# Performance work log

Hardware: AMD Instinct MI355X
Metric: run time of the kernel (lower is better)

The kernel has to match this reference:

```python
import jax, jax.numpy as jnp
import numpy as np

N = 100000
E = 3200000
IN_DIM = 256
HID = 64
NC = 32
K1 = 2  # conv1 propagation steps
EPS = 1e-5


def setup_inputs() -> dict:
    key = jax.random.key(0)
    ks = jax.random.split(key, 8)
    x = jax.random.normal(ks[0], (N, IN_DIM), dtype=jnp.float32)
    src = jax.random.randint(ks[1], (E,), 0, N)
    dst = jax.random.randint(ks[2], (E,), 0, N)
    W1 = jax.random.normal(ks[3], (IN_DIM, HID), dtype=jnp.float32) / np.sqrt(IN_DIM)
    b1 = jnp.zeros((HID,), dtype=jnp.float32)
    gamma = jnp.ones((HID,), dtype=jnp.float32)
    beta = jnp.zeros((HID,), dtype=jnp.float32)
    W2 = jax.random.normal(ks[4], (HID, NC), dtype=jnp.float32) / np.sqrt(HID)
    b2 = jnp.zeros((NC,), dtype=jnp.float32)
    return {"x": x, "src": src, "dst": dst, "W1": W1, "b1": b1,
            "gamma": gamma, "beta": beta, "W2": W2, "b2": b2}


def _gcn_norm(src, dst, n):
    # deg includes self loop (add_self_loops=True): deg[i] = 1 + in-degree
    deg = jax.ops.segment_sum(jnp.ones_like(src, dtype=jnp.float32), dst, num_segments=n) + 1.0
    dinv = jax.lax.rsqrt(deg)
    w_edge = dinv[src] * dinv[dst]      # [E] normalized edge weights
    w_self = dinv * dinv                # [N] self-loop weights (1/deg)
    return w_edge, w_self


def _propagate(h, src, dst, w_edge, w_self, n):
    # out = D^-1/2 (A+I) D^-1/2 h  via gather-scale-scatter
    msg = w_edge[:, None] * h[src]
    agg = jax.ops.segment_sum(msg, dst, num_segments=n)
    return agg + w_self[:, None] * h


def reference(x, src, dst, W1, b1, gamma, beta, W2, b2):
    n = x.shape[0]
    w_edge, w_self = _gcn_norm(src, dst, n)
    # conv1: K-step propagation then linear
    h = x
    for _ in range(K1):
        h = _propagate(h, src, dst, w_edge, w_self, n)
    h = h @ W1 + b1
    # batchnorm (training-mode batch stats over nodes, biased variance)
    mean = jnp.mean(h, axis=0)
    var = jnp.mean(jnp.square(h - mean), axis=0)
    h = (h - mean) * jax.lax.rsqrt(var + EPS) * gamma + beta
    h = jax.nn.selu(h)
    # dropout p=0.0 -> identity
    # conv2: 1-step propagation then linear
    h = _propagate(h, src, dst, w_edge, w_self, n)
    h = h @ W2 + b2
    return jax.nn.log_softmax(h, axis=1)
```

## Files before the change

### kernel.cpp

```cpp
#include <hip/hip_runtime.h>
#include <hip/hip_fp16.h>

#define NN 100000
#define EE 3200000
#define NB 256
#define NPB 391
#define NBLK_A 512
#define CHUNK_A (EE / NBLK_A)

#define OFF_AF   0UL
#define OFF_AH   25600000UL
#define OFF_BH   38400000UL
#define OFF_CNT  (OFF_BH + 65536UL)
#define OFF_LOC  (OFF_CNT + 524288UL)
#define OFF_CSR  51200000UL
#define OFF_RP   64000000UL
#define OFF_DINV 64400384UL
#define OFF_BASE 64808960UL
#define OFF_BN   64813056UL
#define OFF_SS   64813568UL

typedef __attribute__((ext_vector_type(8))) short bf16x8;
typedef __attribute__((ext_vector_type(4))) float f32x4;

__global__ __launch_bounds__(256) void passA2(const int* __restrict__ src, const int* __restrict__ dst,
                                              int* __restrict__ cnt, int* __restrict__ loc,
                                              unsigned* __restrict__ gbuf) {
    __shared__ unsigned ebuf[CHUNK_A];
    __shared__ int hist[NB], cur[NB], sc[NB];
    int t = threadIdx.x, b = blockIdx.x;
    hist[t] = 0;
    __syncthreads();
    int beg = b * CHUNK_A;
    for (int i = t; i < CHUNK_A; i += 256)
        atomicAdd(&hist[dst[beg + i] / NPB], 1);
    __syncthreads();
    int h = hist[t];
    sc[t] = h;
    __syncthreads();
    for (int off = 1; off < 256; off <<= 1) {
        int v = (t >= off) ? sc[t - off] : 0;
        __syncthreads();
        sc[t] += v;
        __syncthreads();
    }
    int ex = sc[t] - h;
    cur[t] = ex;
    loc[b * NB + t] = ex;
    cnt[b * NB + t] = h;
    __syncthreads();
    for (int i = t; i < CHUNK_A; i += 256) {
        int d = dst[beg + i];
        int k = d / NPB;
        int dl = d - k * NPB;
        int p = atomicAdd(&cur[k], 1);
        ebuf[p] = ((unsigned)dl << 17) | (unsigned)src[beg + i];
    }
    __syncthreads();
    for (int i = t; i < CHUNK_A; i += 256)
        gbuf[beg + i] = ebuf[i];
}

__global__ __launch_bounds__(256) void basescan(const int* __restrict__ cnt, int* __restrict__ base,
                                                int* __restrict__ rp) {
    __shared__ int s[256];
    int t = threadIdx.x;
    int v = 0;
    for (int b = 0; b < NBLK_A; ++b) v += cnt[b * NB + t];
    s[t] = v;
    __syncthreads();
    for (int off = 1; off < 256; off <<= 1) {
        int u = (t >= off) ? s[t - off] : 0;
        __syncthreads();
        s[t] += u;
        __syncthreads();
    }
    base[t] = s[t] - v;
    if (t == 255) { base[256] = s[255]; rp[NN] = s[255]; }
}

__global__ __launch_bounds__(512) void passB2(const unsigned* __restrict__ gbuf,
                                              const int* __restrict__ cnt, const int* __restrict__ loc,
                                              const int* __restrict__ base,
                                              int* __restrict__ rp, float* __restrict__ dinv,
                                              int* __restrict__ csr) {
    __shared__ int deg_l[NPB];
    __shared__ int off_l[NPB];
    __shared__ int s[512];
    int k = blockIdx.x, t = threadIdx.x;
    for (int i = t; i < NPB; i += 512) deg_l[i] = 0;
    __syncthreads();
    int n  = cnt[t * NB + k];
    int so = t * CHUNK_A + loc[t * NB + k];
    for (int e = 0; e < n; ++e)
        atomicAdd(&deg_l[gbuf[so + e] >> 17], 1);
    __syncthreads();
    int d0 = (t < NPB) ? deg_l[t] : 0;
    s[t] = d0;
    __syncthreads();
    for (int off = 1; off < 512; off <<= 1) {
        int v = (t >= off) ? s[t - off] : 0;
        __syncthreads();
        s[t] += v;
        __syncthreads();
    }
    if (t < NPB) off_l[t] = s[t] - d0;
    __syncthreads();
    int nodebase = k * NPB;
    int cbase = base[k];
    for (int i = t; i < NPB; i += 512) {
        int node = nodebase + i;
        if (node < NN) {
            rp[node] = cbase + off_l[i];
            dinv[node] = rsqrtf((float)deg_l[i] + 1.0f);
        }
    }
    __syncthreads();
    for (int e = 0; e < n; ++e) {
        unsigned v = gbuf[so + e];
        int p = atomicAdd(&off_l[v >> 17], 1);
        csr[cbase + p] = (int)(v & 0x1FFFFu);
    }
}

__global__ __launch_bounds__(256) void wprep(const float* __restrict__ W1, short* __restrict__ wf) {
    int e = blockIdx.x * 256 + threadIdx.x;
    if (e >= 16384) return;
    int j = e & 7, lane = (e >> 3) & 63, nt = (e >> 9) & 3, ks = e >> 11;
    int k = ks * 32 + (lane >> 4) * 8 + j;
    int col = nt * 16 + (lane & 15);
    float w = W1[k * 64 + col];
    unsigned b = __float_as_uint(w);
    short hi = (short)(b >> 16);
    float hf = __uint_as_float(b & 0xFFFF0000u);
    float lo = w - hf;
    short lov = (short)(__float_as_uint(lo) >> 16);
    wf[((size_t)(ks * 8 + nt * 2 + 0) * 64 + lane) * 8 + j] = hi;
    wf[((size_t)(ks * 8 + nt * 2 + 1) * 64 + lane) * 8 + j] = lov;
}

__global__ __launch_bounds__(256) void gemm1(const float* __restrict__ x, const short* __restrict__ wf,
                                             const float* __restrict__ dinv, __half* __restrict__ Ah) {
    int wid = threadIdx.x >> 6, lane = threadIdx.x & 63;
    int g = blockIdx.x * 4 + wid;
    if (g >= NN / 16) return;
    int lrow = g * 16 + (lane & 15);
    int kgrp = (lane >> 4) * 8;
    const float* xp = x + (size_t)lrow * 256 + kgrp;
    f32x4 acc[4];
    #pragma unroll
    for (int nt = 0; nt < 4; ++nt) acc[nt] = (f32x4){0.f, 0.f, 0.f, 0.f};
    for (int ks = 0; ks < 8; ++ks) {
        float4 f0 = *(const float4*)(xp + ks * 32);
        float4 f1 = *(const float4*)(xp + ks * 32 + 4);
        bf16x8 a_hi, a_lo;
        const float* fp = &f0.x;
        #pragma unroll
        for (int j = 0; j < 8; ++j) {
            float f = (j < 4) ? fp[j] : (&f1.x)[j - 4];
            unsigned b = __float_as_uint(f);
            a_hi[j] = (short)(b >> 16);
            float lo = f - __uint_as_float(b & 0xFFFF0000u);
            a_lo[j] = (short)(__float_as_uint(lo) >> 16);
        }
        const short* wfk = wf + (size_t)(ks * 8) * 64 * 8;
        #pragma unroll
        for (int nt = 0; nt < 4; ++nt) {
            bf16x8 b_hi = *(const bf16x8*)(wfk + ((nt * 2 + 0) * 64 + lane) * 8);
            bf16x8 b_lo = *(const bf16x8*)(wfk + ((nt * 2 + 1) * 64 + lane) * 8);
            acc[nt] = __builtin_amdgcn_mfma_f32_16x16x32_bf16(a_hi, b_hi, acc[nt], 0, 0, 0);
            acc[nt] = __builtin_amdgcn_mfma_f32_16x16x32_bf16(a_hi, b_lo, acc[nt], 0, 0, 0);
            acc[nt] = __builtin_amdgcn_mfma_f32_16x16x32_bf16(a_lo, b_hi, acc[nt], 0, 0, 0);
        }
    }
    int mb = (lane >> 4) * 4;
    #pragma unroll
    for (int reg = 0; reg < 4; ++reg) {
        int row = g * 16 + mb + reg;
        float dv = dinv[row];
        #pragma unroll
        for (int nt = 0; nt < 4; ++nt)
            Ah[(size_t)row * 64 + nt * 16 + (lane & 15)] = __float2half(acc[nt][reg] * dv);
    }
}

template <int P>
__global__ __launch_bounds__(256) void agg64h(const __half* __restrict__ h, __half* __restrict__ outp,
                                              const int* __restrict__ rp, const int* __restrict__ csr,
                                              const float* __restrict__ dinv) {
    int lane = threadIdx.x & 63;
    int node = (blockIdx.x << 2) + (threadIdx.x >> 6);
    if (node >= NN) return;
    int hid = lane >> 5;
    int c2 = (lane & 31) * 2;
    float dd = dinv[node];
    float sfx = 0.f, sfy = 0.f;
    if (hid == 0) {
        __half2 sv = *(const __half2*)(h + (size_t)node * 64 + c2);
        sfx = __half2float(sv.x); sfy = __half2float(sv.y);
    }
    __half2 haccA = __float2half2_rn(0.f);
    __half2 haccB = __float2half2_rn(0.f);
    int beg = rp[node], end = rp[node + 1];
    for (int j0 = beg; j0 < end; j0 += 64) {
        int m = end - j0; if (m > 64) m = 64;
        int s = csr[j0 + (lane < m ? lane : 0)];
        int j = 0;
        for (; j + 15 < m; j += 16) {
            int i0 = __shfl(s, j + hid);
            int i1 = __shfl(s, j + 2 + hid);
            int i2 = __shfl(s, j + 4 + hid);
            int i3 = __shfl(s, j + 6 + hid);
            int i4 = __shfl(s, j + 8 + hid);
            int i5 = __shfl(s, j + 10 + hid);
            int i6 = __shfl(s, j + 12 + hid);
            int i7 = __shfl(s, j + 14 + hid);
            __half2 v0 = *(const __half2*)(h + (size_t)i0 * 64 + c2);
            __half2 v1 = *(const __half2*)(h + (size_t)i1 * 64 + c2);
            __half2 v2 = *(const __half2*)(h + (size_t)i2 * 64 + c2);
            __half2 v3 = *(const __half2*)(h + (size_t)i3 * 64 + c2);
            __half2 v4 = *(const __half2*)(h + (size_t)i4 * 64 + c2);
            __half2 v5 = *(const __half2*)(h + (size_t)i5 * 64 + c2);
            __half2 v6 = *(const __half2*)(h + (size_t)i6 * 64 + c2);
            __half2 v7 = *(const __half2*)(h + (size_t)i7 * 64 + c2);
            __half2 tA = __hadd2(__hadd2(v0, v2), __hadd2(v4, v6));
            __half2 tB = __hadd2(__hadd2(v1, v3), __hadd2(v5, v7));
            haccA = __hadd2(haccA, tA);
            haccB = __hadd2(haccB, tB);
        }
        for (; j + 7 < m; j += 8) {
            int i0 = __shfl(s, j + hid);
            int i1 = __shfl(s, j + 2 + hid);
            int i2 = __shfl(s, j + 4 + hid);
            int i3 = __shfl(s, j + 6 + hid);
            __half2 v0 = *(const __half2*)(h + (size_t)i0 * 64 + c2);
            __half2 v1 = *(const __half2*)(h + (size_t)i1 * 64 + c2);
            __half2 v2 = *(const __half2*)(h + (size_t)i2 * 64 + c2);
            __half2 v3 = *(const __half2*)(h + (size_t)i3 * 64 + c2);
            haccA = __hadd2(haccA, __hadd2(v0, v2));
            haccB = __hadd2(haccB, __hadd2(v1, v3));
        }
        for (; j < m; j += 2) {
            int idx = j + hid;
            int cidx = idx < m ? idx : m - 1;
            int sj = __shfl(s, cidx);
            if (idx < m) {
                __half2 v = *(const __half2*)(h + (size_t)sj * 64 + c2);
                haccA = __hadd2(haccA, v);
            }
        }
    }
    float2 fA = __half22float2(haccA);
    float2 fB = __half22float2(haccB);
    float sx = sfx + fA.x + fB.x;
    float sy = sfy + fA.y + fB.y;
    sx += __shfl(sx, lane ^ 32);
    sy += __shfl(sy, lane ^ 32);
    if (hid == 0) {
        float w = (P == 2) ? dd * dd : dd;
        __half2 o;
        o.x = __float2half(sx * w); o.y = __float2half(sy * w);
        *(__half2*)(outp + (size_t)node * 64 + c2) = o;
    }
}

__global__ __launch_bounds__(256) void agg32f(const __half* __restrict__ U, float* __restrict__ outp,
                                              const int* __restrict__ rp, const int* __restrict__ csr,
                                              const float* __restrict__ dinv, const float* __restrict__ b2) {
    int lane = threadIdx.x & 63;
    int node = (blockIdx.x << 2) + (threadIdx.x >> 6);
    if (node >= NN) return;
    int gid = lane >> 4;
    int c2 = (lane & 15) * 2;
    float dd = dinv[node];
    float sfx = 0.f, sfy = 0.f;
    if (gid == 0) {
        __half2 sv = *(const __half2*)(U + (size_t)node * 32 + c2);
        sfx = __half2float(sv.x); sfy = __half2float(sv.y);
    }
    __half2 hacc = __float2half2_rn(0.f);
    int beg = rp[node], end = rp[node + 1];
    for (int j0 = beg; j0 < end; j0 += 64) {
        int m = end - j0; if (m > 64) m = 64;
        int s = csr[j0 + (lane < m ? lane : 0)];
        int j = 0;
        for (; j + 15 < m; j += 16) {
            int i0 = __shfl(s, j + gid);
            int i1 = __shfl(s, j + 4 + gid);
            int i2 = __shfl(s, j + 8 + gid);
            int i3 = __shfl(s, j + 12 + gid);
            __half2 v0 = *(const __half2*)(U + (size_t)i0 * 32 + c2);
            __half2 v1 = *(const __half2*)(U + (size_t)i1 * 32 + c2);
            __half2 v2 = *(const __half2*)(U + (size_t)i2 * 32 + c2);
            __half2 v3 = *(const __half2*)(U + (size_t)i3 * 32 + c2);
            hacc = __hadd2(hacc, __hadd2(__hadd2(v0, v1), __hadd2(v2, v3)));
        }
        for (; j + 7 < m; j += 8) {
            int i0 = __shfl(s, j + gid);
            int i1 = __shfl(s, j + 4 + gid);
            __half2 v0 = *(const __half2*)(U + (size_t)i0 * 32 + c2);
            __half2 v1 = *(const __half2*)(U + (size_t)i1 * 32 + c2);
            hacc = __hadd2(hacc, __hadd2(v0, v1));
        }
        for (; j < m; j += 4) {
            int idx = j + gid;
            int cidx = idx < m ? idx : m - 1;
            int sj = __shfl(s, cidx);
            if (idx < m) {
                __half2 v = *(const __half2*)(U + (size_t)sj * 32 + c2);
                hacc = __hadd2(hacc, v);
            }
        }
    }
    float2 fh = __half22float2(hacc);
    float ax = sfx + fh.x, ay = sfy + fh.y;
    ax += __shfl(ax, lane ^ 16); ay += __shfl(ay, lane ^ 16);
    ax += __shfl(ax, lane ^ 32); ay += __shfl(ay, lane ^ 32);
    float v0 = ax * dd + b2[c2];
    float v1 = ay * dd + b2[c2 + 1];
    float mx = fmaxf(v0, v1);
    mx = fmaxf(mx, __shfl_xor(mx, 1));
    mx = fmaxf(mx, __shfl_xor(mx, 2));
    mx = fmaxf(mx, __shfl_xor(mx, 4));
    mx = fmaxf(mx, __shfl_xor(mx, 8));
    float sum = __expf(v0 - mx) + __expf(v1 - mx);
    sum += __shfl_xor(sum, 1);
    sum += __shfl_xor(sum, 2);
    sum += __shfl_xor(sum, 4);
    sum += __shfl_xor(sum, 8);
    if (gid == 0) {
        float ls = __logf(sum);
        *(float2*)(outp + (size_t)node * 32 + c2) = make_float2(v0 - mx - ls, v1 - mx - ls);
    }
}

__global__ __launch_bounds__(256) void bn_stats(const __half* __restrict__ A, float* __restrict__ bn) {
    int t = threadIdx.x;
    int c = t & 63, rg = t >> 6;
    float s = 0.f, sq = 0.f;
    for (int r = blockIdx.x * 4 + rg; r < NN; r += gridDim.x * 4) {
        float v = __half2float(A[(size_t)r * 64 + c]);
        s += v; sq += v * v;
    }
    __shared__ float ls[256], lq[256];
    ls[t] = s; lq[t] = sq;
    __syncthreads();
    if (t < 64) {
        float S = ls[t] + ls[t + 64] + ls[t + 128] + ls[t + 192];
        float Q = lq[t] + lq[t + 64] + lq[t + 128] + lq[t + 192];
        atomicAdd(&bn[t], S);
        atomicAdd(&bn[64 + t], Q);
    }
}

__global__ void bn_final(const float* __restrict__ bn, const float* __restrict__ gamma,
                         const float* __restrict__ beta, float* __restrict__ ss) {
    int c = threadIdx.x;
    float mean = bn[c] / (float)NN;
    float var = bn[64 + c] / (float)NN - mean * mean;
    float sc = gamma[c] * rsqrtf(var + 1e-5f);
    ss[c] = sc;
    ss[64 + c] = beta[c] - mean * sc;
}

__global__ __launch_bounds__(256) void gemm2(const __half* __restrict__ A, const float* __restrict__ W2,
                                             const float* __restrict__ ss, const float* __restrict__ dinv,
                                             __half* __restrict__ U) {
    __shared__ float w2s[64 * 32];
    __shared__ float sc[64], sh[64];
    for (int i = threadIdx.x; i < 512; i += 256)
        ((float4*)w2s)[i] = ((const float4*)W2)[i];
    if (threadIdx.x < 64) {
        sc[threadIdx.x] = ss[threadIdx.x];
        sh[threadIdx.x] = ss[64 + threadIdx.x];
    }
    __syncthreads();
    const float SELU_S = 1.0507009873554805f;
    const float SELU_AS = 1.7580993408473766f;
    int lane = threadIdx.x & 31, grp = threadIdx.x >> 5;
    int node = blockIdx.x * 8 + grp;
    if (node >= NN) return;
    const __half* Ar = A + (size_t)node * 64;
    float v0 = __half2float(Ar[lane]);
    float v1 = __half2float(Ar[lane + 32]);
    v0 = v0 * sc[lane] + sh[lane];
    v1 = v1 * sc[lane + 32] + sh[lane + 32];
    v0 = v0 > 0.f ? SELU_S * v0 : SELU_AS * (__expf(v0) - 1.0f);
    v1 = v1 > 0.f ? SELU_S * v1 : SELU_AS * (__expf(v1) - 1.0f);
    float acc = 0.f;
    #pragma unroll
    for (int j = 0; j < 32; ++j) {
        acc += __shfl(v0, j, 32) * w2s[j * 32 + lane];
        acc += __shfl(v1, j, 32) * w2s[(j + 32) * 32 + lane];
    }
    U[(size_t)node * 32 + lane] = __float2half(dinv[node] * acc);
}

extern "C" void kernel_launch(void* const* d_in, const int* in_sizes, int n_in,
                              void* d_out, int out_size, void* d_ws, size_t ws_size,
                              hipStream_t stream) {
    const float* x     = (const float*)d_in[0];
    const int*   src   = (const int*)d_in[1];
    const int*   dst   = (const int*)d_in[2];
    const float* W1    = (const float*)d_in[3];
    const float* gamma = (const float*)d_in[5];
    const float* beta  = (const float*)d_in[6];
    const float* W2    = (const float*)d_in[7];
    const float* b2    = (const float*)d_in[8];
    float* out = (float*)d_out;

    char* ws = (char*)d_ws;
    __half*   Af   = (__half*)(ws + OFF_AF);
    unsigned* gbuf = (unsigned*)(ws + OFF_AF);
    __half*   Ah   = (__half*)(ws + OFF_AH);
    __half*   Bh   = (__half*)(ws + OFF_BH);
    short*    wf   = (short*)(ws + OFF_BH);
    __half*   Uh   = (__half*)(ws + OFF_BH);
    int*      cnt  = (int*)(ws + OFF_CNT);
    int*      loc  = (int*)(ws + OFF_LOC);
    int*      csr  = (int*)(ws + OFF_CSR);
    int*      rp   = (int*)(ws + OFF_RP);
    float*    dinv = (float*)(ws + OFF_DINV);
    int*      base = (int*)(ws + OFF_BASE);
    float*    bn   = (float*)(ws + OFF_BN);
    float*    ssb  = (float*)(ws + OFF_SS);

    hipMemsetAsync(bn, 0, 128 * sizeof(float), stream);

    wprep<<<64, 256, 0, stream>>>(W1, wf);

    passA2<<<NBLK_A, 256, 0, stream>>>(src, dst, cnt, loc, gbuf);
    basescan<<<1, 256, 0, stream>>>(cnt, base, rp);
    passB2<<<NB, 512, 0, stream>>>(gbuf, cnt, loc, base, rp, dinv, csr);

    gemm1<<<(NN / 16 + 3) / 4, 256, 0, stream>>>(x, wf, dinv, Ah);
    agg64h<2><<<NN / 4, 256, 0, stream>>>(Ah, Bh, rp, csr, dinv);
    agg64h<1><<<NN / 4, 256, 0, stream>>>(Bh, Af, rp, csr, dinv);

    bn_stats<<<1024, 256, 0, stream>>>(Af, bn);
    bn_final<<<1, 64, 0, stream>>>(bn, gamma, beta, ssb);

    gemm2<<<NN / 8, 256, 0, stream>>>(Af, W2, ssb, dinv, Uh);
    agg32f<<<NN / 4, 256, 0, stream>>>(Uh, out, rp, csr, dinv, b2);
}
```

Before: 352.7 us.

## Split 64-wide features into 8 column slices for sliced neighbor aggregation

Stores the hidden activations as 8 planes of 8 halves per node instead of rows of 64. Each aggregation block now handles one slice: every lane takes one edge and does a 16-byte gather, and a wave reduction sums the partial results. This meant to make the per-slice working set (1.6 MB) fit in cache and to raise memory-level parallelism, at the cost of 8x more blocks, reading the CSR once per slice, and a shuffle reduction per node. The gemm1 store and the BN-stats and gemm2 loads are rewritten for the new layout, and they now do scattered 2-byte accesses.

```diff
diff --git a/kernel.cpp b/kernel.cpp
--- a/kernel.cpp
+++ b/kernel.cpp
@@ -3,6 +3,7 @@
 
 #define NN 100000
 #define EE 3200000
+#define NN8 (NN * 8)
 #define NB 256
 #define NPB 391
 #define NBLK_A 512
@@ -22,6 +23,9 @@
 
 typedef __attribute__((ext_vector_type(8))) short bf16x8;
 typedef __attribute__((ext_vector_type(4))) float f32x4;
+
+__device__ __forceinline__ __half2 u2h2(unsigned u) { return *(__half2*)&u; }
+__device__ __forceinline__ unsigned h22u(__half2 h) { return *(unsigned*)&h; }
 
 __global__ __launch_bounds__(256) void passA2(const int* __restrict__ src, const int* __restrict__ dst,
                                               int* __restrict__ cnt, int* __restrict__ loc,
@@ -179,88 +183,59 @@
         int row = g * 16 + mb + reg;
         float dv = dinv[row];
         #pragma unroll
-        for (int nt = 0; nt < 4; ++nt)
-            Ah[(size_t)row * 64 + nt * 16 + (lane & 15)] = __float2half(acc[nt][reg] * dv);
+        for (int nt = 0; nt < 4; ++nt) {
+            int col = nt * 16 + (lane & 15);
+            Ah[(size_t)(col >> 3) * NN8 + (size_t)row * 8 + (col & 7)] =
+                __float2half(acc[nt][reg] * dv);
+        }
     }
 }
 
 template <int P>
-__global__ __launch_bounds__(256) void agg64h(const __half* __restrict__ h, __half* __restrict__ outp,
+__global__ __launch_bounds__(256) void agg64s(const __half* __restrict__ h, __half* __restrict__ outp,
                                               const int* __restrict__ rp, const int* __restrict__ csr,
                                               const float* __restrict__ dinv) {
-    int lane = threadIdx.x & 63;
-    int node = (blockIdx.x << 2) + (threadIdx.x >> 6);
-    if (node >= NN) return;
-    int hid = lane >> 5;
-    int c2 = (lane & 31) * 2;
-    float dd = dinv[node];
-    float sfx = 0.f, sfy = 0.f;
-    if (hid == 0) {
-        __half2 sv = *(const __half2*)(h + (size_t)node * 64 + c2);
-        sfx = __half2float(sv.x); sfy = __half2float(sv.y);
-    }
-    __half2 haccA = __float2half2_rn(0.f);
-    __half2 haccB = __float2half2_rn(0.f);
-    int beg = rp[node], end = rp[node + 1];
+    int wid = threadIdx.x >> 6, lane = threadIdx.x & 63;
+    int slice = blockIdx.x & 7;
+    int node = (blockIdx.x >> 3) * 4 + wid;
+    const __half* hs = h + (size_t)slice * NN8;
+    __half2 a0 = __float2half2_rn(0.f), a1 = a0, a2 = a0, a3 = a0;
+    int beg = __builtin_nontemporal_load(rp + node);
+    int end = __builtin_nontemporal_load(rp + node + 1);
     for (int j0 = beg; j0 < end; j0 += 64) {
-        int m = end - j0; if (m > 64) m = 64;
-        int s = csr[j0 + (lane < m ? lane : 0)];
-        int j = 0;
-        for (; j + 15 < m; j += 16) {
-            int i0 = __shfl(s, j + hid);
-            int i1 = __shfl(s, j + 2 + hid);
-            int i2 = __shfl(s, j + 4 + hid);
-            int i3 = __shfl(s, j + 6 + hid);
-            int i4 = __shfl(s, j + 8 + hid);
-            int i5 = __shfl(s, j + 10 + hid);
-            int i6 = __shfl(s, j + 12 + hid);
-            int i7 = __shfl(s, j + 14 + hid);
-            __half2 v0 = *(const __half2*)(h + (size_t)i0 * 64 + c2);
-            __half2 v1 = *(const __half2*)(h + (size_t)i1 * 64 + c2);
-            __half2 v2 = *(const __half2*)(h + (size_t)i2 * 64 + c2);
-            __half2 v3 = *(const __half2*)(h + (size_t)i3 * 64 + c2);
-            __half2 v4 = *(const __half2*)(h + (size_t)i4 * 64 + c2);
-            __half2 v5 = *(const __half2*)(h + (size_t)i5 * 64 + c2);
-            __half2 v6 = *(const __half2*)(h + (size_t)i6 * 64 + c2);
-            __half2 v7 = *(const __half2*)(h + (size_t)i7 * 64 + c2);
-            __half2 tA = __hadd2(__hadd2(v0, v2), __hadd2(v4, v6));
-            __half2 tB = __hadd2(__hadd2(v1, v3), __hadd2(v5, v7));
-            haccA = __hadd2(haccA, tA);
-            haccB = __hadd2(haccB, tB);
-        }
-        for (; j + 7 < m; j += 8) {
-            int i0 = __shfl(s, j + hid);
-            int i1 = __shfl(s, j + 2 + hid);
-            int i2 = __shfl(s, j + 4 + hid);
-            int i3 = __shfl(s, j + 6 + hid);
-            __half2 v0 = *(const __half2*)(h + (size_t)i0 * 64 + c2);
-            __half2 v1 = *(const __half2*)(h + (size_t)i1 * 64 + c2);
-            __half2 v2 = *(const __half2*)(h + (size_t)i2 * 64 + c2);
-            __half2 v3 = *(const __half2*)(h + (size_t)i3 * 64 + c2);
-            haccA = __hadd2(haccA, __hadd2(v0, v2));
-            haccB = __hadd2(haccB, __hadd2(v1, v3));
-        }
-        for (; j < m; j += 2) {
-            int idx = j + hid;
-            int cidx = idx < m ? idx : m - 1;
-            int sj = __shfl(s, cidx);
-            if (idx < m) {
-                __half2 v = *(const __half2*)(h + (size_t)sj * 64 + c2);
-                haccA = __hadd2(haccA, v);
-            }
-        }
-    }
-    float2 fA = __half22float2(haccA);
-    float2 fB = __half22float2(haccB);
-    float sx = sfx + fA.x + fB.x;
-    float sy = sfy + fA.y + fB.y;
-    sx += __shfl(sx, lane ^ 32);
-    sy += __shfl(sy, lane ^ 32);
-    if (hid == 0) {
+        int m = end - j0;
+        if (lane < m) {
+            int sj = __builtin_nontemporal_load(csr + j0 + lane);
+            uint4 v = *(const uint4*)(hs + (size_t)sj * 8);
+            a0 = __hadd2(a0, u2h2(v.x));
+            a1 = __hadd2(a1, u2h2(v.y));
+            a2 = __hadd2(a2, u2h2(v.z));
+            a3 = __hadd2(a3, u2h2(v.w));
+        }
+    }
+    #pragma unroll
+    for (int off = 32; off; off >>= 1) {
+        a0 = __hadd2(a0, u2h2(__shfl_xor(h22u(a0), off)));
+        a1 = __hadd2(a1, u2h2(__shfl_xor(h22u(a1), off)));
+        a2 = __hadd2(a2, u2h2(__shfl_xor(h22u(a2), off)));
+        a3 = __hadd2(a3, u2h2(__shfl_xor(h22u(a3), off)));
+    }
+    if (lane == 0) {
+        uint4 sv = *(const uint4*)(hs + (size_t)node * 8);
+        float dd = dinv[node];
         float w = (P == 2) ? dd * dd : dd;
-        __half2 o;
-        o.x = __float2half(sx * w); o.y = __float2half(sy * w);
-        *(__half2*)(outp + (size_t)node * 64 + c2) = o;
+        float2 f0 = __half22float2(a0), f1 = __half22float2(a1);
+        float2 f2 = __half22float2(a2), f3 = __half22float2(a3);
+        float2 s0 = __half22float2(u2h2(sv.x)), s1 = __half22float2(u2h2(sv.y));
+        float2 s2 = __half22float2(u2h2(sv.z)), s3 = __half22float2(u2h2(sv.w));
+        __half2 o0, o1, o2, o3;
+        o0.x = __float2half((f0.x + s0.x) * w); o0.y = __float2half((f0.y + s0.y) * w);
+        o1.x = __float2half((f1.x + s1.x) * w); o1.y = __float2half((f1.y + s1.y) * w);
+        o2.x = __float2half((f2.x + s2.x) * w); o2.y = __float2half((f2.y + s2.y) * w);
+        o3.x = __float2half((f3.x + s3.x) * w); o3.y = __float2half((f3.y + s3.y) * w);
+        uint4 ov;
+        ov.x = h22u(o0); ov.y = h22u(o1); ov.z = h22u(o2); ov.w = h22u(o3);
+        *(uint4*)(outp + (size_t)slice * NN8 + (size_t)node * 8) = ov;
     }
 }
 
@@ -337,9 +312,11 @@
 __global__ __launch_bounds__(256) void bn_stats(const __half* __restrict__ A, float* __restrict__ bn) {
     int t = threadIdx.x;
     int c = t & 63, rg = t >> 6;
+    size_t plane = (size_t)(c >> 3) * NN8;
+    int cl = c & 7;
     float s = 0.f, sq = 0.f;
     for (int r = blockIdx.x * 4 + rg; r < NN; r += gridDim.x * 4) {
-        float v = __half2float(A[(size_t)r * 64 + c]);
+        float v = __half2float(A[plane + (size_t)r * 8 + cl]);
         s += v; sq += v * v;
     }
     __shared__ float ls[256], lq[256];
@@ -380,11 +357,11 @@
     int lane = threadIdx.x & 31, grp = threadIdx.x >> 5;
     int node = blockIdx.x * 8 + grp;
     if (node >= NN) return;
-    const __half* Ar = A + (size_t)node * 64;
-    float v0 = __half2float(Ar[lane]);
-    float v1 = __half2float(Ar[lane + 32]);
-    v0 = v0 * sc[lane] + sh[lane];
-    v1 = v1 * sc[lane + 32] + sh[lane + 32];
+    int c0 = lane, c1 = lane + 32;
+    float v0 = __half2float(A[(size_t)(c0 >> 3) * NN8 + (size_t)node * 8 + (c0 & 7)]);
+    float v1 = __half2float(A[(size_t)(c1 >> 3) * NN8 + (size_t)node * 8 + (c1 & 7)]);
+    v0 = v0 * sc[c0] + sh[c0];
+    v1 = v1 * sc[c1] + sh[c1];
     v0 = v0 > 0.f ? SELU_S * v0 : SELU_AS * (__expf(v0) - 1.0f);
     v1 = v1 > 0.f ? SELU_S * v1 : SELU_AS * (__expf(v1) - 1.0f);
     float acc = 0.f;
@@ -434,8 +411,8 @@
     passB2<<<NB, 512, 0, stream>>>(gbuf, cnt, loc, base, rp, dinv, csr);
 
     gemm1<<<(NN / 16 + 3) / 4, 256, 0, stream>>>(x, wf, dinv, Ah);
-    agg64h<2><<<NN / 4, 256, 0, stream>>>(Ah, Bh, rp, csr, dinv);
-    agg64h<1><<<NN / 4, 256, 0, stream>>>(Bh, Af, rp, csr, dinv);
+    agg64s<2><<<(NN / 4) * 8, 256, 0, stream>>>(Ah, Bh, rp, csr, dinv);
+    agg64s<1><<<(NN / 4) * 8, 256, 0, stream>>>(Bh, Af, rp, csr, dinv);
 
     bn_stats<<<1024, 256, 0, stream>>>(Af, bn);
     bn_final<<<1, 64, 0, stream>>>(bn, gamma, beta, ssb);
```

New measurement: 774.3 us. +119.6%, slower.
